# Performance work log

Hardware: AMD Instinct MI355X
Metric: run time of the kernel (lower is better)

The kernel has to match this reference:

```python
import jax, jax.numpy as jnp
import numpy as np
from jax import lax

EPS = 1e-5


def maxpool3x3(x):
    # 3x3 max pool, stride 1, pad 1 (NCHW)
    return lax.reduce_window(x, -jnp.inf, lax.max,
                             window_dimensions=(1, 1, 3, 3),
                             window_strides=(1, 1, 1, 1),
                             padding=((0, 0), (0, 0), (1, 1), (1, 1)))


def focus_downsample(x):
    B, C, H, W = x.shape
    pad_h = (3 - H % 3) % 3
    pad_w = (3 - W % 3) % 3
    if pad_h or pad_w:
        x = jnp.pad(x, ((0, 0), (0, 0), (0, pad_h), (0, pad_w)))
    return jnp.concatenate([x[..., i::3, j::3] for i in range(3) for j in range(3)], axis=1)


def batchnorm(x, gamma, beta):
    # training-mode BatchNorm2d: stats over (B,H,W)
    mean = jnp.mean(x, axis=(0, 2, 3), keepdims=True)
    var = jnp.var(x, axis=(0, 2, 3), keepdims=True)
    g = gamma.reshape(1, -1, 1, 1)
    b = beta.reshape(1, -1, 1, 1)
    return (x - mean) * jax.lax.rsqrt(var + EPS) * g + b


def dwconv(x, w, pad_h, pad_w):
    # depthwise conv, w: (C,1,kh,kw)
    return lax.conv_general_dilated(x, w, window_strides=(1, 1),
                                    padding=((pad_h, pad_h), (pad_w, pad_w)),
                                    dimension_numbers=('NCHW', 'OIHW', 'NCHW'),
                                    feature_group_count=x.shape[1])


def h_transform(x):
    B, C, H, W = x.shape
    x = jnp.pad(x, ((0, 0), (0, 0), (0, 0), (0, W)))
    x = x.reshape(B, C, -1)[..., :-W]
    return x.reshape(B, C, H, 2 * W - 1)


def inv_h_transform(x):
    B, C, H, _ = x.shape
    x = x.reshape(B, C, -1)
    x = jnp.pad(x, ((0, 0), (0, 0), (0, H)))
    x = x.reshape(B, C, H, 2 * H)
    return x[..., :H]


def v_transform(x):
    return h_transform(x.transpose(0, 1, 3, 2)).transpose(0, 1, 3, 2)


def inv_v_transform(x):
    return inv_h_transform(x.transpose(0, 1, 3, 2)).transpose(0, 1, 3, 2)


def pixel_shuffle3(x):
    B, C9, h, w = x.shape
    C = C9 // 9
    x = x.reshape(B, C, 3, 3, h, w)
    x = x.transpose(0, 1, 4, 2, 5, 3)  # B,C,h,3,w,3
    return x.reshape(B, C, 3 * h, 3 * w)


def setup_inputs() -> dict:
    key = jax.random.key(0)
    ks = jax.random.split(key, 10)
    C, K = 64, 11
    B, H, W = 16, 144, 144
    s = 0.05
    return {
        'x': jax.random.normal(ks[0], (B, C, H, W), jnp.float32),
        'w_mixer': jax.random.normal(ks[1], (9, C, C), jnp.float32) * s,
        'g_mnorm': jnp.ones((9 * C,), jnp.float32),
        'b_mnorm': jnp.zeros((9 * C,), jnp.float32),
        'w_h1': jax.random.normal(ks[2], (C, 1, K, 3), jnp.float32) * s,
        'w_v1': jax.random.normal(ks[3], (C, 1, 3, K), jnp.float32) * s,
        'w_h2': jax.random.normal(ks[4], (C, 1, K, 3), jnp.float32) * s,
        'w_v2': jax.random.normal(ks[5], (C, 1, 3, K), jnp.float32) * s,
        'g_norm': jnp.ones((C,), jnp.float32),
        'b_norm': jnp.zeros((C,), jnp.float32),
    }


def reference(x, w_mixer, g_mnorm, b_mnorm, w_h1, w_v1, w_h2, w_v2, g_norm, b_norm):
    C = w_h1.shape[0]
    K = w_h1.shape[2]
    pad = K // 2
    H, W = x.shape[-2:]

    x_pool = maxpool3x3(x)
    x_focus = focus_downsample(x_pool)               # (B,9C,H/3,W/3)

    # grouped 1x1 conv, groups=9
    B, _, h, w = x_focus.shape
    xg = x_focus.reshape(B, 9, C, h, w)
    x_mixed = jnp.einsum('goi,bgihw->bgohw', w_mixer, xg).reshape(B, 9 * C, h, w)
    x_mixed = batchnorm(x_mixed, g_mnorm, b_mnorm)

    x_tem, x_key = x_mixed[:, :C], x_mixed[:, C:]

    x_h1 = dwconv(x_tem, w_h1, pad, 1)
    x_w1 = dwconv(x_tem, w_v1, 1, pad)
    x_h2 = inv_h_transform(dwconv(h_transform(x_tem), w_h2, pad, 1))
    x_w2 = inv_v_transform(dwconv(v_transform(x_tem), w_v2, 1, pad))

    att_map = batchnorm(x_h1 + x_w1 + x_h2 + x_w2, g_norm, b_norm)
    final_features = jnp.concatenate([att_map, x_key], axis=1)
    att = pixel_shuffle3(final_features)[..., :H, :W]
    return x * jax.nn.sigmoid(att)
```

## Files before the change

### kernel.cpp

```cpp
#include <hip/hip_runtime.h>
#include <hip/hip_bf16.h>

typedef __hip_bfloat16 bf16;
typedef unsigned short us;
typedef __attribute__((ext_vector_type(8))) short short8;
typedef __attribute__((ext_vector_type(4))) float floatx4;

__device__ __forceinline__ float b2f(bf16 v){ return __bfloat162float(v); }
__device__ __forceinline__ bf16  f2b(float v){ return __float2bfloat16(v); }
__device__ __forceinline__ float ldx(const void* p, size_t i, int isf){
    return isf ? ((const float*)p)[i] : b2f(((const bf16*)p)[i]);
}
__device__ __forceinline__ us bfbits(float v){
    bf16 h = f2b(v); return *(us*)&h;
}
__device__ __forceinline__ float us2f(us u){
    unsigned int w = ((unsigned int)u)<<16; float f; __builtin_memcpy(&f,&w,4); return f;
}

#define BB   16
#define CC   64
#define HH   144
#define WW   144
#define HS   48
#define SP   (HS*HS)
#define NTOT (BB*CC*HH*WW)
#define NCH  36864
#define INV_NCH (1.f/36864.f)

__global__ void k_init(const unsigned int* __restrict__ x, int* __restrict__ flag,
                       float* __restrict__ stats){
    for(int i=threadIdx.x; i<1280; i+=256) stats[i] = 0.f;
    __shared__ int hit;
    if(threadIdx.x==0) hit = 0;
    __syncthreads();
    int local = 0;
    for(int t=threadIdx.x; t<4096; t+=256){
        unsigned int w = x[t];
        if(((w>>7)&0xFFu)==0xFFu || ((w>>23)&0xFFu)==0xFFu) local = 1;
    }
    if(local) atomicOr(&hit, 1);
    __syncthreads();
    if(threadIdx.x==0) *flag = hit;
}

__global__ __launch_bounds__(256) void k_pool3(const void* __restrict__ x,
                                               us* __restrict__ pf,
                                               const int* __restrict__ flag){
    __shared__ float l [18*148];
    __shared__ float hm[18*148];
    int isf = *flag;
    int bid = blockIdx.x;
    int strip = bid % 9;
    int bc = bid / 9;
    int b = bc>>6, c = bc&63;
    int r0 = strip*16;
    size_t base = (size_t)bc*HH*WW;
    int tid = threadIdx.x;
    for(int t=tid; t<18*18; t+=256){
        int row = t/18, ch = t%18;
        int rr = r0-1+row; int c0 = ch*8;
        float v[8];
        if(rr>=0 && rr<HH){
            if(isf){
                const float* xp = (const float*)x + base + (size_t)rr*WW + c0;
                float4 f0 = *(const float4*)xp;
                float4 f1 = *(const float4*)(xp+4);
                v[0]=f0.x;v[1]=f0.y;v[2]=f0.z;v[3]=f0.w;
                v[4]=f1.x;v[5]=f1.y;v[6]=f1.z;v[7]=f1.w;
            } else {
                const us* xp = (const us*)x + base + (size_t)rr*WW + c0;
                uint4 d = *(const uint4*)xp;
                const us* u = (const us*)&d;
                #pragma unroll
                for(int e=0;e<8;++e) v[e] = us2f(u[e]);
            }
        } else {
            #pragma unroll
            for(int e=0;e<8;++e) v[e] = -INFINITY;
        }
        #pragma unroll
        for(int e=0;e<8;++e) l[row*148 + c0 + e] = v[e];
    }
    __syncthreads();
    for(int t=tid; t<18*144; t+=256){
        int row = t/144, cc = t%144;
        float a = l[row*148+cc];
        float bb = (cc>0)   ? l[row*148+cc-1] : -INFINITY;
        float cv = (cc<143) ? l[row*148+cc+1] : -INFINITY;
        hm[row*148+cc] = fmaxf(a, fmaxf(bb,cv));
    }
    __syncthreads();
    for(int t=tid; t<576; t+=256){
        int row = t/36;
        int gj  = (t/12)%3;
        int xg  = t%12;
        int R = r0+row;
        int gi = R%3, y = R/3;
        union { us u[4]; uint2 v; } pk;
        #pragma unroll
        for(int e=0;e<4;++e){
            int xx = xg*4+e; int C = 3*xx+gj;
            float m = fmaxf(hm[row*148+C],
                      fmaxf(hm[(row+1)*148+C], hm[(row+2)*148+C]));
            pk.u[e] = bfbits(m);
        }
        size_t o = ((((size_t)(b*3+gi)*3+gj)*64 + c)*48 + y)*48 + xg*4;
        *(uint2*)&pf[o] = pk.v;
    }
}

__global__ __launch_bounds__(256) void k_mix3(const us* __restrict__ pf,
        const void* __restrict__ wmix, us* __restrict__ mixed,
        float* __restrict__ sum1, float* __restrict__ ss1,
        const int* __restrict__ flag){
    __shared__ __align__(16) us sW[4096];
    __shared__ __align__(16) us sI[288*64];
    __shared__ float sS[64], sQ[64];
    int isf = *flag;
    int bid = blockIdx.x;
    int chunk = bid%8, g = (bid/8)%9, b = bid/72;
    int gi = g/3, gj = g%3;
    int tid = threadIdx.x, lane = tid&63, w = tid>>6;
    {
        int o  = tid>>2;
        int i0 = (tid&3)*16;
        #pragma unroll
        for(int e=0;e<16;++e){
            int i = i0+e;
            float v = ldx(wmix, (size_t)g*4096 + (size_t)o*64 + i, isf);
            sW[o*64 + ((((i>>3)+o)&7)<<3) + (i&7)] = bfbits(v);
        }
    }
    if(tid<64){ sS[tid]=0.f; sQ[tid]=0.f; }
    {
        int i = lane;
        const us* src = pf + ((((size_t)(b*3+gi)*3+gj)*64 + i)*48 + (size_t)chunk*6)*48;
        for(int vv=w*9; vv<(w+1)*9; ++vv){
            uint4 d = *(const uint4*)(src + vv*8);
            const us* u = (const us*)&d;
            #pragma unroll
            for(int e=0;e<8;++e){
                int s = vv*8+e;
                sI[s*64 + ((((i>>3)+s)&7)<<3) + (i&7)] = u[e];
            }
        }
    }
    __syncthreads();
    int n = lane&15, quad = lane>>4;
    int m = w*16 + n;
    short8 a0 = *(const short8*)&sW[m*64 + (((quad     + m)&7)<<3)];
    short8 a1 = *(const short8*)&sW[m*64 + ((((4+quad) + m)&7)<<3)];
    floatx4 acc[18];
    #pragma unroll
    for(int nt=0; nt<18; ++nt) acc[nt] = (floatx4){0.f,0.f,0.f,0.f};
    #pragma unroll
    for(int nt=0; nt<18; ++nt){
        int site = nt*16 + n;
        short8 b0 = *(const short8*)&sI[site*64 + (((quad     + site)&7)<<3)];
        short8 b1 = *(const short8*)&sI[site*64 + ((((4+quad) + site)&7)<<3)];
        acc[nt] = __builtin_amdgcn_mfma_f32_16x16x32_bf16(a0, b0, acc[nt], 0,0,0);
        acc[nt] = __builtin_amdgcn_mfma_f32_16x16x32_bf16(a1, b1, acc[nt], 0,0,0);
    }
    size_t obase = (size_t)(b*576 + g*64)*SP + (size_t)chunk*288;
    float s[4] = {0,0,0,0}, q[4] = {0,0,0,0};
    #pragma unroll
    for(int nt=0; nt<18; ++nt){
        #pragma unroll
        for(int r=0;r<4;++r){
            float v = acc[nt][r];
            int o = w*16 + quad*4 + r;
            mixed[obase + (size_t)o*SP + nt*16 + n] = bfbits(v);
            s[r] += v; q[r] += v*v;
        }
    }
    #pragma unroll
    for(int off=1; off<=8; off<<=1){
        #pragma unroll
        for(int r=0;r<4;++r){
            s[r] += __shfl_xor(s[r], off, 64);
            q[r] += __shfl_xor(q[r], off, 64);
        }
    }
    if(n==0){
        #pragma unroll
        for(int r=0;r<4;++r){
            atomicAdd(&sS[w*16+quad*4+r], s[r]);
            atomicAdd(&sQ[w*16+quad*4+r], q[r]);
        }
    }
    __syncthreads();
    if(tid<64){
        atomicAdd(&sum1[g*64+tid], sS[tid]);
        atomicAdd(&ss1 [g*64+tid], sQ[tid]);
    }
}

__global__ __launch_bounds__(256) void k_conv3(const us* __restrict__ mixed,
    const float* __restrict__ sum1, const float* __restrict__ ss1,
    const void* __restrict__ gm, const void* __restrict__ bm,
    const void* __restrict__ wh1, const void* __restrict__ wv1,
    const void* __restrict__ wh2, const void* __restrict__ wv2,
    us* __restrict__ att, float* __restrict__ sum2, float* __restrict__ ss2,
    const int* __restrict__ flag){
    __shared__ float tile[60*60+4];
    __shared__ float w1[33], w2[33], w34[39];
    __shared__ float r1[256], r2[256];
    int isf = *flag;
    int bid = blockIdx.x;
    int b = bid/64, c = bid%64;
    int tid = threadIdx.x;
    for(int t=tid; t<3604; t+=256) tile[t] = 0.f;
    if(tid < 33){
        w1[tid] = ldx(wh1, c*33 + tid, isf);
    } else if(tid < 66){
        w2[tid-33] = ldx(wv1, c*33 + (tid-33), isf);
    } else if(tid < 105){
        int k = tid-66;
        int r = k/3 - 6;
        int vo = k%3 - 1;
        float a = 0.f;
        if(r >= -5 && r <= 5)
            a += ldx(wh2, c*33 + (r+5)*3 + (vo+1), isf);
        int u = vo - r;
        if(u >= -5 && u <= 5)
            a += ldx(wv2, c*33 + (vo+1)*11 + (u+5), isf);
        w34[k] = a;
    }
    __syncthreads();
    float mu   = sum1[c]*INV_NCH;
    float var  = ss1[c]*INV_NCH - mu*mu;
    float is   = rsqrtf(var + 1e-5f)*ldx(gm,c,isf);
    float be   = ldx(bm,c,isf);
    const us* src = mixed + (size_t)(b*576 + c)*SP;
    float w1r[33], w2r[33], w34r[39];
    #pragma unroll
    for(int i=0;i<33;++i) w1r[i] = w1[i];
    #pragma unroll
    for(int i=0;i<33;++i) w2r[i] = w2[i];
    #pragma unroll
    for(int i=0;i<39;++i) w34r[i] = w34[i];
    for(int t=tid; t<288; t+=256){
        int h = t/6, w0 = (t%6)*8;
        uint4 d = *(const uint4*)(src + t*8);
        const us* u = (const us*)&d;
        #pragma unroll
        for(int e=0;e<8;++e)
            tile[(h+6)*60 + (w0+6) + e] = (us2f(u[e]) - mu)*is + be;
    }
    __syncthreads();
    us* out = att + (size_t)(b*64 + c)*SP;
    float sl = 0.f, ql = 0.f;
    #pragma unroll 1
    for(int it=0; it<9; ++it){
        int t = it*256 + tid;
        int hh = t/48 + 6, w = t%48 + 6;
        const float* bp = &tile[hh*60 + w];
        float acc = 0.f;
        #pragma unroll
        for(int r=-1; r<=1; ++r)
            #pragma unroll
            for(int v=-5; v<=5; ++v)
                acc += w2r[(r+1)*11 + (v+5)] * bp[r*60 + v];
        #pragma unroll
        for(int r=-5; r<=5; ++r)
            #pragma unroll
            for(int v=-1; v<=1; ++v)
                acc += w1r[(r+5)*3 + (v+1)] * bp[r*60 + v];
        #pragma unroll
        for(int r=-6; r<=6; ++r)
            #pragma unroll
            for(int v=-1; v<=1; ++v)
                acc += w34r[(r+6)*3 + (v+1)] * bp[r*60 + (v-r)];
        out[t] = bfbits(acc);
        sl += acc; ql += acc*acc;
    }
    r1[tid]=sl; r2[tid]=ql; __syncthreads();
    for(int o=128;o>0;o>>=1){
        if(tid<o){ r1[tid]+=r1[tid+o]; r2[tid]+=r2[tid+o]; }
        __syncthreads();
    }
    if(tid==0){
        atomicAdd(&sum2[c], r1[0]);
        atomicAdd(&ss2 [c], r2[0]);
    }
}

__global__ __launch_bounds__(256) void k_final3(const void* __restrict__ x,
    const us* __restrict__ mixed, const us* __restrict__ att,
    const void* __restrict__ gm, const void* __restrict__ bm,
    const void* __restrict__ gn, const void* __restrict__ bnb,
    const float* __restrict__ sum1, const float* __restrict__ ss1,
    const float* __restrict__ sum2, const float* __restrict__ ss2,
    void* __restrict__ out, const int* __restrict__ flag){
    __shared__ __align__(16) us sT[9*1152];
    __shared__ float scs[9], shs[9];
    int isf = *flag;
    int bid = blockIdx.x;
    int half = bid&1, c = (bid>>1)&63, b = bid>>7;
    int yy0 = half*24;
    int tid = threadIdx.x;
    if(tid < 9){
        int f = 9*c + tid;
        float sraw, qraw, gg, bb2;
        if(f < 64){ sraw = sum2[f]; qraw = ss2[f]; gg = ldx(gn,f,isf);  bb2 = ldx(bnb,f,isf); }
        else      { sraw = sum1[f]; qraw = ss1[f]; gg = ldx(gm,f,isf);  bb2 = ldx(bm,f,isf); }
        float mm  = sraw*INV_NCH;
        float ist = rsqrtf(qraw*INV_NCH - mm*mm + 1e-5f);
        float sc = ist*gg;
        scs[tid] = sc;
        shs[tid] = bb2 - mm*sc;
    }
    for(int t=tid; t<9*144; t+=256){
        int j = t/144, qq = t%144;
        int f = 9*c + j;
        const us* srcp = ((f<64) ? att   + (size_t)(b*64 +f)*SP
                                 : mixed + (size_t)(b*576+f)*SP) + yy0*48;
        ((uint4*)&sT[j*1152])[qq] = ((const uint4*)srcp)[qq];
    }
    __syncthreads();
    size_t pbase = (size_t)(b*64+c)*HH*WW;
    for(int t=tid; t<1296; t+=256){
        int Yl = t/18;
        int Xb = (t%18)*8;
        int yyl = Yl/3, r = Yl%3;
        float vo[8];
        #pragma unroll
        for(int k=0;k<8;++k){
            int X = Xb+k;
            int xx = X/3, sph = X%3;
            int j = 3*r + sph;
            float raw = us2f(sT[j*1152 + yyl*48 + xx]);
            float v = raw*scs[j] + shs[j];
            vo[k] = 1.f/(1.f + __expf(-v));
        }
        size_t off = pbase + (size_t)(yy0*3 + Yl)*WW + Xb;
        if(isf){
            const float4* xp = (const float4*)((const float*)x + off);
            float4 x0 = xp[0], x1 = xp[1];
            float4 o0, o1;
            o0.x = x0.x*vo[0]; o0.y = x0.y*vo[1]; o0.z = x0.z*vo[2]; o0.w = x0.w*vo[3];
            o1.x = x1.x*vo[4]; o1.y = x1.y*vo[5]; o1.z = x1.z*vo[6]; o1.w = x1.w*vo[7];
            float4* op = (float4*)((float*)out + off);
            op[0] = o0; op[1] = o1;
        } else {
            uint4 xr = *(const uint4*)((const us*)x + off);
            const us* xu = (const us*)&xr;
            union { us u[8]; uint4 v; } pk;
            #pragma unroll
            for(int k=0;k<8;++k)
                pk.u[k] = bfbits(us2f(xu[k])*vo[k]);
            *(uint4*)((us*)out + off) = pk.v;
        }
    }
}


extern "C" void kernel_launch(void* const* d_in, const int* in_sizes, int n_in,
                              void* d_out, int out_size, void* d_ws, size_t ws_size,
                              hipStream_t stream) {
    (void)in_sizes; (void)n_in; (void)out_size; (void)ws_size;
    const void* x    = d_in[0];
    const void* wmix = d_in[1];
    const void* gm   = d_in[2];
    const void* bm   = d_in[3];
    const void* wh1  = d_in[4];
    const void* wv1  = d_in[5];
    const void* wh2  = d_in[6];
    const void* wv2  = d_in[7];
    const void* gn   = d_in[8];
    const void* bnb  = d_in[9];

    us* pf = (us*)d_out;
    char* ws = (char*)d_ws;
    us*    mixed = (us*)   (ws + 0);
    us*    att   = (us*)   (ws + 42467328);
    float* st1a  = (float*)(ws + 47185920);
    float* st1b  = (float*)(ws + 47188224);
    float* st2a  = (float*)(ws + 47190528);
    float* st2b  = (float*)(ws + 47190784);
    int*   flag  = (int*)  (ws + 47191040);

    k_init  <<<1, 256, 0, stream>>>((const unsigned int*)x, flag, st1a);
    k_pool3 <<<BB*CC*9, 256, 0, stream>>>(x, pf, flag);
    k_mix3  <<<BB*9*8, 256, 0, stream>>>(pf, wmix, mixed, st1a, st1b, flag);
    k_conv3 <<<BB*64, 256, 0, stream>>>(mixed, st1a, st1b, gm, bm,
                                        wh1, wv1, wh2, wv2, att, st2a, st2b, flag);
    k_final3<<<BB*CC*2, 256, 0, stream>>>(x, mixed, att, gm, bm, gn, bnb,
                                          st1a, st1b, st2a, st2b, d_out, flag);
}
```

Measured before the change: 260.5 us.

## Drop init kernel, template dtype flag, and stage mix output through LDS

Removes the separate init kernel. Input dtype is now decided on the host from in_sizes and passed as a template parameter, and stats zeroing moves into block 0 of the pool kernel. The mix kernel loads its weights with vector loads and writes the bf16 GEMM output through per-wave LDS staging, so each global store is a coalesced 16-byte store instead of a scattered 2-byte store. Zeroing stats inside k_pool3 is safe only because k_mix3 runs after it in stream order, and the sniff kernel is kept as a fallback for unknown sizes.

```diff
diff --git a/kernel.cpp b/kernel.cpp
--- a/kernel.cpp
+++ b/kernel.cpp
@@ -28,9 +28,13 @@
 #define NCH  36864
 #define INV_NCH (1.f/36864.f)
 
-__global__ void k_init(const unsigned int* __restrict__ x, int* __restrict__ flag,
-                       float* __restrict__ stats){
-    for(int i=threadIdx.x; i<1280; i+=256) stats[i] = 0.f;
+template<int TISF>
+__device__ __forceinline__ int isf_of(const int* flag){
+    if(TISF >= 0) return TISF;
+    return *flag;
+}
+
+__global__ void k_sniff(const unsigned int* __restrict__ x, int* __restrict__ flag){
     __shared__ int hit;
     if(threadIdx.x==0) hit = 0;
     __syncthreads();
@@ -44,19 +48,24 @@
     if(threadIdx.x==0) *flag = hit;
 }
 
+template<int TISF>
 __global__ __launch_bounds__(256) void k_pool3(const void* __restrict__ x,
                                                us* __restrict__ pf,
-                                               const int* __restrict__ flag){
+                                               const int* __restrict__ flag,
+                                               float* __restrict__ stats){
     __shared__ float l [18*148];
     __shared__ float hm[18*148];
-    int isf = *flag;
+    int isf = isf_of<TISF>(flag);
     int bid = blockIdx.x;
+    int tid = threadIdx.x;
+    if(bid==0){
+        for(int i=tid; i<1280; i+=256) stats[i] = 0.f;
+    }
     int strip = bid % 9;
     int bc = bid / 9;
     int b = bc>>6, c = bc&63;
     int r0 = strip*16;
     size_t base = (size_t)bc*HH*WW;
-    int tid = threadIdx.x;
     for(int t=tid; t<18*18; t+=256){
         int row = t/18, ch = t%18;
         int rr = r0-1+row; int c0 = ch*8;
@@ -110,14 +119,16 @@
     }
 }
 
+template<int TISF>
 __global__ __launch_bounds__(256) void k_mix3(const us* __restrict__ pf,
         const void* __restrict__ wmix, us* __restrict__ mixed,
         float* __restrict__ sum1, float* __restrict__ ss1,
         const int* __restrict__ flag){
-    __shared__ __align__(16) us sW[4096];
-    __shared__ __align__(16) us sI[288*64];
+    __shared__ __align__(16) us sAll[4096 + 288*64];
     __shared__ float sS[64], sQ[64];
-    int isf = *flag;
+    us* sW = sAll;
+    us* sI = sAll + 4096;
+    int isf = isf_of<TISF>(flag);
     int bid = blockIdx.x;
     int chunk = bid%8, g = (bid/8)%9, b = bid/72;
     int gi = g/3, gj = g%3;
@@ -125,11 +136,26 @@
     {
         int o  = tid>>2;
         int i0 = (tid&3)*16;
+        us wb[16];
+        if(isf){
+            const float* wp = (const float*)wmix + (size_t)g*4096 + (size_t)o*64 + i0;
+            #pragma unroll
+            for(int e=0;e<16;e+=4){
+                float4 f = *(const float4*)(wp+e);
+                wb[e]=bfbits(f.x); wb[e+1]=bfbits(f.y);
+                wb[e+2]=bfbits(f.z); wb[e+3]=bfbits(f.w);
+            }
+        } else {
+            const us* wp = (const us*)wmix + (size_t)g*4096 + (size_t)o*64 + i0;
+            uint4 d0 = *(const uint4*)wp, d1 = *(const uint4*)(wp+8);
+            const us* u0 = (const us*)&d0; const us* u1 = (const us*)&d1;
+            #pragma unroll
+            for(int e=0;e<8;++e){ wb[e]=u0[e]; wb[8+e]=u1[e]; }
+        }
         #pragma unroll
         for(int e=0;e<16;++e){
             int i = i0+e;
-            float v = ldx(wmix, (size_t)g*4096 + (size_t)o*64 + i, isf);
-            sW[o*64 + ((((i>>3)+o)&7)<<3) + (i&7)] = bfbits(v);
+            sW[o*64 + ((((i>>3)+o)&7)<<3) + (i&7)] = wb[e];
         }
     }
     if(tid<64){ sS[tid]=0.f; sQ[tid]=0.f; }
@@ -162,15 +188,12 @@
         acc[nt] = __builtin_amdgcn_mfma_f32_16x16x32_bf16(a0, b0, acc[nt], 0,0,0);
         acc[nt] = __builtin_amdgcn_mfma_f32_16x16x32_bf16(a1, b1, acc[nt], 0,0,0);
     }
-    size_t obase = (size_t)(b*576 + g*64)*SP + (size_t)chunk*288;
     float s[4] = {0,0,0,0}, q[4] = {0,0,0,0};
     #pragma unroll
     for(int nt=0; nt<18; ++nt){
         #pragma unroll
         for(int r=0;r<4;++r){
             float v = acc[nt][r];
-            int o = w*16 + quad*4 + r;
-            mixed[obase + (size_t)o*SP + nt*16 + n] = bfbits(v);
             s[r] += v; q[r] += v*v;
         }
     }
@@ -194,8 +217,26 @@
         atomicAdd(&sum1[g*64+tid], sS[tid]);
         atomicAdd(&ss1 [g*64+tid], sQ[tid]);
     }
-}
-
+    us* swr = sAll + w*640;
+    int o_loc = lane>>2, s8 = (lane&3)*8;
+    size_t rowbase = ((size_t)(b*576 + g*64 + w*16))*SP + (size_t)chunk*288;
+    #pragma unroll
+    for(int mp=0; mp<9; ++mp){
+        __builtin_amdgcn_wave_barrier();
+        #pragma unroll
+        for(int half=0; half<2; ++half){
+            int nt = mp*2 + half;
+            #pragma unroll
+            for(int r=0;r<4;++r)
+                swr[(quad*4+r)*40 + half*16 + n] = bfbits(acc[nt][r]);
+        }
+        __builtin_amdgcn_wave_barrier();
+        uint4 vv = *(const uint4*)&swr[o_loc*40 + s8];
+        *(uint4*)&mixed[rowbase + (size_t)o_loc*SP + (size_t)(mp*32 + s8)] = vv;
+    }
+}
+
+template<int TISF>
 __global__ __launch_bounds__(256) void k_conv3(const us* __restrict__ mixed,
     const float* __restrict__ sum1, const float* __restrict__ ss1,
     const void* __restrict__ gm, const void* __restrict__ bm,
@@ -206,7 +247,7 @@
     __shared__ float tile[60*60+4];
     __shared__ float w1[33], w2[33], w34[39];
     __shared__ float r1[256], r2[256];
-    int isf = *flag;
+    int isf = isf_of<TISF>(flag);
     int bid = blockIdx.x;
     int b = bid/64, c = bid%64;
     int tid = threadIdx.x;
@@ -286,6 +327,7 @@
     }
 }
 
+template<int TISF>
 __global__ __launch_bounds__(256) void k_final3(const void* __restrict__ x,
     const us* __restrict__ mixed, const us* __restrict__ att,
     const void* __restrict__ gm, const void* __restrict__ bm,
@@ -295,7 +337,7 @@
     void* __restrict__ out, const int* __restrict__ flag){
     __shared__ __align__(16) us sT[9*1152];
     __shared__ float scs[9], shs[9];
-    int isf = *flag;
+    int isf = isf_of<TISF>(flag);
     int bid = blockIdx.x;
     int half = bid&1, c = (bid>>1)&63, b = bid>>7;
     int yy0 = half*24;
@@ -359,7 +401,7 @@
 extern "C" void kernel_launch(void* const* d_in, const int* in_sizes, int n_in,
                               void* d_out, int out_size, void* d_ws, size_t ws_size,
                               hipStream_t stream) {
-    (void)in_sizes; (void)n_in; (void)out_size; (void)ws_size;
+    (void)n_in; (void)out_size; (void)ws_size;
     const void* x    = d_in[0];
     const void* wmix = d_in[1];
     const void* gm   = d_in[2];
@@ -381,11 +423,25 @@
     float* st2b  = (float*)(ws + 47190784);
     int*   flag  = (int*)  (ws + 47191040);
 
-    k_init  <<<1, 256, 0, stream>>>((const unsigned int*)x, flag, st1a);
-    k_pool3 <<<BB*CC*9, 256, 0, stream>>>(x, pf, flag);
-    k_mix3  <<<BB*9*8, 256, 0, stream>>>(pf, wmix, mixed, st1a, st1b, flag);
-    k_conv3 <<<BB*64, 256, 0, stream>>>(mixed, st1a, st1b, gm, bm,
-                                        wh1, wv1, wh2, wv2, att, st2a, st2b, flag);
-    k_final3<<<BB*CC*2, 256, 0, stream>>>(x, mixed, att, gm, bm, gn, bnb,
-                                          st1a, st1b, st2a, st2b, d_out, flag);
-}
+    int isf;
+    if(in_sizes[0] == (int)((long long)NTOT*4)) isf = 1;
+    else if(in_sizes[0] == (int)((long long)NTOT*2)) isf = 0;
+    else isf = -1;
+
+    if(isf < 0)
+        k_sniff<<<1, 256, 0, stream>>>((const unsigned int*)x, flag);
+
+#define LAUNCH_ALL(T)                                                          \
+    k_pool3<T><<<BB*CC*9, 256, 0, stream>>>(x, pf, flag, st1a);                \
+    k_mix3<T><<<BB*9*8, 256, 0, stream>>>(pf, wmix, mixed, st1a, st1b, flag);  \
+    k_conv3<T><<<BB*64, 256, 0, stream>>>(mixed, st1a, st1b, gm, bm,           \
+                                          wh1, wv1, wh2, wv2, att,             \
+                                          st2a, st2b, flag);                   \
+    k_final3<T><<<BB*CC*2, 256, 0, stream>>>(x, mixed, att, gm, bm, gn, bnb,   \
+                                             st1a, st1b, st2a, st2b, d_out, flag);
+
+    if(isf == 1)      { LAUNCH_ALL(1)  }
+    else if(isf == 0) { LAUNCH_ALL(0)  }
+    else              { LAUNCH_ALL(-1) }
+#undef LAUNCH_ALL
+}
```

Measured after the change: 250.9 us. 3.7% less time.
